# Kernel optimization log

Hardware: AMD Instinct MI355X
Metric: run time of the kernel (lower is better)

Reference implementation:

```python
import jax, jax.numpy as jnp
import numpy as np

D_MODEL = 512
NUM_HEADS = 8
DEPTH = D_MODEL // NUM_HEADS
MAX_SEQ = 2048
B, L = 4, 1024


def setup_inputs() -> dict:
    key = jax.random.key(0)
    ks = jax.random.split(key, 13)
    s = 0.02
    return {
        "v": jax.random.normal(ks[0], (B, L, D_MODEL), jnp.float32),
        "k": jax.random.normal(ks[1], (B, L, D_MODEL), jnp.float32),
        "q": jax.random.normal(ks[2], (B, L, D_MODEL), jnp.float32),
        "mask": jnp.zeros((1, 1, L, L), jnp.float32),
        "wq_w": jax.random.normal(ks[3], (D_MODEL, D_MODEL), jnp.float32) * s,
        "wq_b": jnp.zeros((D_MODEL,), jnp.float32),
        "wk_w": jax.random.normal(ks[4], (D_MODEL, D_MODEL), jnp.float32) * s,
        "wk_b": jnp.zeros((D_MODEL,), jnp.float32),
        "wv_w": jax.random.normal(ks[5], (D_MODEL, D_MODEL), jnp.float32) * s,
        "wv_b": jnp.zeros((D_MODEL,), jnp.float32),
        "wo_w": jax.random.normal(ks[6], (D_MODEL, D_MODEL), jnp.float32) * s,
        "wo_b": jnp.zeros((D_MODEL,), jnp.float32),
        "pos_emb": jax.random.normal(ks[7], (MAX_SEQ, DEPTH), jnp.float32) * s,
    }


def _split_heads(x, batch):
    # [B, L, d_model] -> [B, H, L, depth]
    return x.reshape(batch, -1, NUM_HEADS, DEPTH).transpose(0, 2, 1, 3)


def reference(v, k, q, mask, wq_w, wq_b, wk_w, wk_b, wv_w, wv_b, wo_w, wo_b, pos_emb):
    batch, l_q, _ = q.shape
    qh = _split_heads(q @ wq_w + wq_b, batch)   # [B,H,Lq,depth]
    kh = _split_heads(k @ wk_w + wk_b, batch)   # [B,H,Lk,depth]
    vh = _split_heads(v @ wv_w + wv_b, batch)   # [B,H,Lk,depth]
    l_k = kh.shape[2]

    # relative position embedding slice: last l_q rows of pos_emb -> [Lq, depth]
    e = pos_emb[max(0, MAX_SEQ - l_q):, :]
    qe = jnp.einsum('nhld,md->nhlm', qh, e)     # [B,H,Lq,Lq]

    # upper-left triangular masking: keep entries with i + j >= Lq - 1
    keep = (jnp.arange(l_q)[:, None] + jnp.arange(l_q)[None, :]) >= (l_q - 1)
    qe = qe * keep.astype(qe.dtype)

    # skew trick: pad left on last dim, reshape [L, L+1]->[L+1, L], drop first row
    padded = jnp.pad(qe, ((0, 0), (0, 0), (0, 0), (1, 0)))
    srel = padded.reshape(batch, NUM_HEADS, l_q + 1, l_q)[:, :, 1:, :]  # [B,H,Lq,Lq]
    if l_k > l_q:
        srel = jnp.pad(srel, ((0, 0), (0, 0), (0, 0), (0, l_k - l_q)))
    elif l_k < l_q:
        srel = srel[..., :l_k]

    scale = 1.0 / jnp.sqrt(jnp.asarray(DEPTH, qh.dtype))
    logits = (jnp.einsum('nhld,nhmd->nhlm', qh, kh) + srel) * scale
    logits = logits + mask * (-1e9)
    attn = jax.nn.softmax(logits, axis=-1)      # [B,H,Lq,Lk]
    ctx = jnp.einsum('nhlm,nhmd->nhld', attn, vh)
    ctx = ctx.transpose(0, 2, 1, 3).reshape(batch, l_q, D_MODEL)
    out = ctx @ wo_w + wo_b
    return out, attn
```

## Files before the change

### kernel.cpp

```cpp
#include <hip/hip_runtime.h>

typedef __attribute__((ext_vector_type(4))) float f32x4;
typedef __attribute__((ext_vector_type(8))) short s16x8;
typedef __attribute__((ext_vector_type(4))) unsigned short u16x4;

__device__ inline unsigned short f2bf(float f) {
  unsigned int u = __builtin_bit_cast(unsigned int, f);
  u += 0x7fff + ((u >> 16) & 1);
  return (unsigned short)(u >> 16);
}
__device__ inline float bf2f(unsigned short u) {
  return __builtin_bit_cast(float, (unsigned int)u << 16);
}

__device__ __forceinline__ void async16(const void* g, void* s) {
  __builtin_amdgcn_global_load_lds(
      (const __attribute__((address_space(1))) unsigned int*)g,
      (__attribute__((address_space(3))) unsigned int*)s, 16, 0, 0);
}

__global__ __launch_bounds__(256) void cast_kernel(
    const float* __restrict__ v, const float* __restrict__ k, const float* __restrict__ q,
    const float* __restrict__ wq, const float* __restrict__ wk, const float* __restrict__ wv,
    const float* __restrict__ wo, const float* __restrict__ pos,
    unsigned short* __restrict__ qbf, unsigned short* __restrict__ kbf,
    unsigned short* __restrict__ vbf, unsigned short* __restrict__ wqT,
    unsigned short* __restrict__ wkT, unsigned short* __restrict__ wvT,
    unsigned short* __restrict__ woT, unsigned short* __restrict__ ebf) {
  int seg = blockIdx.y;
  int tid = blockIdx.x * blockDim.x + threadIdx.x;
  int stride = gridDim.x * blockDim.x;
  if (seg < 3) {
    const float* src = seg == 0 ? q : (seg == 1 ? k : v);
    unsigned short* dst = seg == 0 ? qbf : (seg == 1 ? kbf : vbf);
    for (int i = tid; i < 4096 * 512 / 4; i += stride) {
      f32x4 x = *(const f32x4*)&src[i * 4];
      u16x4 o = {f2bf(x[0]), f2bf(x[1]), f2bf(x[2]), f2bf(x[3])};
      *(u16x4*)&dst[i * 4] = o;
    }
  } else if (seg < 7) {
    const float* src = seg == 3 ? wq : seg == 4 ? wk : seg == 5 ? wv : wo;
    unsigned short* dst = seg == 3 ? wqT : seg == 4 ? wkT : seg == 5 ? wvT : woT;
    for (int i = tid; i < 512 * 128; i += stride) {
      int n = i >> 7, k0 = (i & 127) * 4;
      u16x4 o = {f2bf(src[(k0 + 0) * 512 + n]), f2bf(src[(k0 + 1) * 512 + n]),
                 f2bf(src[(k0 + 2) * 512 + n]), f2bf(src[(k0 + 3) * 512 + n])};
      *(u16x4*)&dst[n * 512 + k0] = o;
    }
  } else {
    for (int i = tid; i < 1024 * 64 / 4; i += stride) {
      f32x4 x = *(const f32x4*)&pos[1024 * 64 + i * 4];
      u16x4 o = {f2bf(x[0]), f2bf(x[1]), f2bf(x[2]), f2bf(x[3])};
      *(u16x4*)&ebf[i * 4] = o;
    }
  }
}

__device__ __forceinline__ void gemm_main(
    const unsigned short* __restrict__ A, const unsigned short* __restrict__ Bt,
    unsigned short* As, unsigned short* Bs, int r0, int c0, int tid,
    f32x4 acc[4][4]) {
  int lane = tid & 63, w = tid >> 6;
  int wr = w >> 1, wc = w & 1;
  int frow = lane & 15, kg = lane >> 4;
  for (int k0 = 0; k0 < 512; k0 += 32) {
#pragma unroll
    for (int j = 0; j < 2; ++j) {
      int t = tid + j * 256;
      int row = t >> 2, col = (t & 3) * 8;
      *(s16x8*)&As[row * 32 + col] = *(const s16x8*)&A[(size_t)(r0 + row) * 512 + k0 + col];
      *(s16x8*)&Bs[row * 32 + col] = *(const s16x8*)&Bt[(size_t)(c0 + row) * 512 + k0 + col];
    }
    __syncthreads();
    s16x8 af[4], bfr[4];
#pragma unroll
    for (int mi = 0; mi < 4; ++mi) af[mi] = *(s16x8*)&As[(wr * 64 + mi * 16 + frow) * 32 + kg * 8];
#pragma unroll
    for (int ni = 0; ni < 4; ++ni) bfr[ni] = *(s16x8*)&Bs[(wc * 64 + ni * 16 + frow) * 32 + kg * 8];
#pragma unroll
    for (int mi = 0; mi < 4; ++mi)
#pragma unroll
      for (int ni = 0; ni < 4; ++ni)
        acc[mi][ni] = __builtin_amdgcn_mfma_f32_16x16x32_bf16(af[mi], bfr[ni], acc[mi][ni], 0, 0, 0);
    __syncthreads();
  }
}

__global__ __launch_bounds__(256, 2) void proj3_kernel(
    const unsigned short* __restrict__ qbf, const unsigned short* __restrict__ kbf,
    const unsigned short* __restrict__ vbf, const unsigned short* __restrict__ wqT,
    const unsigned short* __restrict__ wkT, const unsigned short* __restrict__ wvT,
    const float* __restrict__ wq_b, const float* __restrict__ wk_b,
    const float* __restrict__ wv_b, unsigned short* __restrict__ qhw,
    unsigned short* __restrict__ khw, unsigned short* __restrict__ vhT) {
  __shared__ unsigned short As[128 * 32];
  __shared__ unsigned short Bs[128 * 32];
  int z = blockIdx.z;
  const unsigned short* A = z == 0 ? qbf : z == 1 ? kbf : vbf;
  const unsigned short* Bt = z == 0 ? wqT : z == 1 ? wkT : wvT;
  const float* bias = z == 0 ? wq_b : z == 1 ? wk_b : wv_b;
  unsigned short* outp = z == 0 ? qhw : z == 1 ? khw : vhT;
  int r0 = blockIdx.x * 128, c0 = blockIdx.y * 128;
  int tid = threadIdx.x;
  int lane = tid & 63, w = tid >> 6;
  int wr = w >> 1, wc = w & 1;
  int frow = lane & 15, kg = lane >> 4;
  f32x4 acc[4][4] = {};
  gemm_main(A, Bt, As, Bs, r0, c0, tid, acc);
#pragma unroll
  for (int ni = 0; ni < 4; ++ni) {
    int gc = c0 + wc * 64 + ni * 16 + frow;
    float bi = bias[gc];
#pragma unroll
    for (int mi = 0; mi < 4; ++mi) {
#pragma unroll
      for (int reg = 0; reg < 4; ++reg) {
        int gr = r0 + wr * 64 + mi * 16 + kg * 4 + reg;
        float val = acc[mi][ni][reg] + bi;
        if (z != 2) {
          outp[(size_t)((gr >> 10) * 8 + (gc >> 6)) * 65536 +
               (size_t)(gr & 1023) * 64 + (gc & 63)] = f2bf(val);
        } else {
          outp[(size_t)((gr >> 10) * 8 + (gc >> 6)) * 65536 +
               (size_t)(gc & 63) * 1024 + (gr & 1023)] = f2bf(val);
        }
      }
    }
  }
}

__global__ __launch_bounds__(256, 2) void gemm_out_kernel(
    const unsigned short* __restrict__ A, const unsigned short* __restrict__ Bt,
    const float* __restrict__ bias, float* __restrict__ outp) {
  __shared__ unsigned short As[128 * 32];
  __shared__ unsigned short Bs[128 * 32];
  int r0 = blockIdx.x * 128, c0 = blockIdx.y * 128;
  int tid = threadIdx.x;
  int lane = tid & 63, w = tid >> 6;
  int wr = w >> 1, wc = w & 1;
  int frow = lane & 15, kg = lane >> 4;
  f32x4 acc[4][4] = {};
  gemm_main(A, Bt, As, Bs, r0, c0, tid, acc);
#pragma unroll
  for (int ni = 0; ni < 4; ++ni) {
    int gc = c0 + wc * 64 + ni * 16 + frow;
    float bi = bias[gc];
#pragma unroll
    for (int mi = 0; mi < 4; ++mi)
#pragma unroll
      for (int reg = 0; reg < 4; ++reg) {
        int gr = r0 + wr * 64 + mi * 16 + kg * 4 + reg;
        outp[(size_t)gr * 512 + gc] = acc[mi][ni][reg] + bi;
      }
  }
}

__global__ __launch_bounds__(256, 2) void attn_kernel(
    const unsigned short* __restrict__ qh, const unsigned short* __restrict__ kh,
    const unsigned short* __restrict__ vhT, const unsigned short* __restrict__ ebf,
    const float* __restrict__ mask, float* __restrict__ attn_out,
    unsigned short* __restrict__ ctx) {
  __shared__ unsigned short S[16 * 1024];
  __shared__ unsigned short KV[2][8192];
  __shared__ float redmax[4][16], redsum[4][16];
  int nh = blockIdx.y;
  int l0 = blockIdx.x * 16;
  int tid = threadIdx.x;
  int lane = tid & 63, w = tid >> 6;
  int frow = lane & 15, kg = lane >> 4;

  auto sp = [&](int r, int c) -> unsigned short* {
    int byte = (r << 11) + (c << 1);
    byte ^= (r & 7) << 4;
    return (unsigned short*)((char*)S + byte);
  };

  auto stageKE = [&](const unsigned short* srcbase, int buf) {
#pragma unroll
    for (int i = 0; i < 4; ++i) {
      int u = (w * 4 + i) * 64 + lane;
      int row = u >> 3, pp = u & 7;
      async16(srcbase + (size_t)row * 64 + (size_t)((pp ^ (row & 7)) * 8),
              &KV[buf][(w * 4 + i) * 512]);
    }
  };
  auto stageV = [&](const unsigned short* srcbase, int c, int buf) {
#pragma unroll
    for (int i = 0; i < 4; ++i) {
      int u = (w * 4 + i) * 64 + lane;
      int row = u >> 4, pp = u & 15;
      int p = (pp & 8) | ((pp ^ (row & 7)) & 7);
      async16(srcbase + (size_t)row * 1024 + c * 128 + p * 8,
              &KV[buf][(w * 4 + i) * 512]);
    }
  };

  const unsigned short* qbase = qh + ((size_t)nh * 1024 + l0 + frow) * 64 + kg * 8;
  s16x8 qf0 = *(const s16x8*)(qbase);
  s16x8 qf1 = *(const s16x8*)(qbase + 32);

  int cmin = 1008 - l0;
  int cstart = cmin >> 7;
  stageKE(ebf + (size_t)cstart * 8192, cstart & 1);
  for (int c = cstart; c < 8; ++c) {
    int buf = c & 1;
    if (c < 7) {
      stageKE(ebf + (size_t)(c + 1) * 8192, buf ^ 1);
      asm volatile("s_waitcnt vmcnt(4)" ::: "memory");
    } else {
      asm volatile("s_waitcnt vmcnt(0)" ::: "memory");
    }
    __builtin_amdgcn_s_barrier();
    __builtin_amdgcn_sched_barrier(0);
#pragma unroll
    for (int tt = 0; tt < 2; ++tt) {
      int j0 = c * 128 + (w * 2 + tt) * 16;
      if (j0 + 15 < cmin) continue;
      int lr = (w * 2 + tt) * 16 + frow;
      const char* base = (const char*)&KV[buf][0] + lr * 128;
      s16x8 b0 = *(const s16x8*)(base + ((kg ^ (lr & 7)) << 4));
      s16x8 b1 = *(const s16x8*)(base + (((4 + kg) ^ (lr & 7)) << 4));
      f32x4 a = {};
      a = __builtin_amdgcn_mfma_f32_16x16x32_bf16(b0, qf0, a, 0, 0, 0);
      a = __builtin_amdgcn_mfma_f32_16x16x32_bf16(b1, qf1, a, 0, 0, 0);
      u16x4 pk = {f2bf(a[0]), f2bf(a[1]), f2bf(a[2]), f2bf(a[3])};
      *(u16x4*)sp(frow, j0 + kg * 4) = pk;
    }
    __builtin_amdgcn_s_barrier();
    __builtin_amdgcn_sched_barrier(0);
  }
  __syncthreads();

  f32x4 lg[16];
  stageKE(kh + (size_t)nh * 65536, 0);
#pragma unroll
  for (int c = 0; c < 8; ++c) {
    int buf = c & 1;
    if (c < 7) {
      stageKE(kh + (size_t)nh * 65536 + (size_t)(c + 1) * 8192, buf ^ 1);
      asm volatile("s_waitcnt vmcnt(4)" ::: "memory");
    } else {
      asm volatile("s_waitcnt vmcnt(0)" ::: "memory");
    }
    __builtin_amdgcn_s_barrier();
    __builtin_amdgcn_sched_barrier(0);
#pragma unroll
    for (int tt = 0; tt < 2; ++tt) {
      int lr = (w * 2 + tt) * 16 + frow;
      const char* base = (const char*)&KV[buf][0] + lr * 128;
      s16x8 b0 = *(const s16x8*)(base + ((kg ^ (lr & 7)) << 4));
      s16x8 b1 = *(const s16x8*)(base + (((4 + kg) ^ (lr & 7)) << 4));
      f32x4 a = {};
      a = __builtin_amdgcn_mfma_f32_16x16x32_bf16(b0, qf0, a, 0, 0, 0);
      a = __builtin_amdgcn_mfma_f32_16x16x32_bf16(b1, qf1, a, 0, 0, 0);
      lg[c * 2 + tt] = a;
    }
    __builtin_amdgcn_s_barrier();
    __builtin_amdgcn_sched_barrier(0);
  }

  int lq = l0 + frow;
#pragma unroll
  for (int c = 0; c < 8; ++c) {
#pragma unroll
    for (int tt = 0; tt < 2; ++tt) {
      int t = c * 2 + tt;
      int m0k = c * 128 + (w * 2 + tt) * 16 + kg * 4;
      f32x4 mk = *(const f32x4*)&mask[(size_t)lq * 1024 + m0k];
#pragma unroll
      for (int reg = 0; reg < 4; ++reg) {
        int m = m0k + reg;
        float srel = (m <= lq) ? bf2f(*sp(frow, 1023 + m - lq)) : 0.f;
        lg[t][reg] = (lg[t][reg] + srel) * 0.125f + mk[reg] * -1e9f;
      }
    }
  }

  f32x4 vmax = lg[0];
#pragma unroll
  for (int t = 1; t < 16; ++t) {
#pragma unroll
    for (int reg = 0; reg < 4; ++reg) vmax[reg] = fmaxf(vmax[reg], lg[t][reg]);
  }
  float mx = fmaxf(fmaxf(vmax[0], vmax[1]), fmaxf(vmax[2], vmax[3]));
  mx = fmaxf(mx, __shfl_xor(mx, 16));
  mx = fmaxf(mx, __shfl_xor(mx, 32));
  float s = 0.f;
#pragma unroll
  for (int t = 0; t < 16; ++t) {
#pragma unroll
    for (int reg = 0; reg < 4; ++reg) {
      lg[t][reg] = __expf(lg[t][reg] - mx);
      s += lg[t][reg];
    }
  }
  s += __shfl_xor(s, 16);
  s += __shfl_xor(s, 32);
  if (lane < 16) {
    redmax[w][lane] = mx;
    redsum[w][lane] = s;
  }
  __syncthreads();

  float gmax = fmaxf(fmaxf(redmax[0][frow], redmax[1][frow]),
                     fmaxf(redmax[2][frow], redmax[3][frow]));
  float gsum = redsum[0][frow] * __expf(redmax[0][frow] - gmax) +
               redsum[1][frow] * __expf(redmax[1][frow] - gmax) +
               redsum[2][frow] * __expf(redmax[2][frow] - gmax) +
               redsum[3][frow] * __expf(redmax[3][frow] - gmax);
  float fac = __expf(mx - gmax) / gsum;

  size_t arow = ((size_t)nh * 1024 + lq) * 1024;
#pragma unroll
  for (int c = 0; c < 8; ++c) {
#pragma unroll
    for (int tt = 0; tt < 2; ++tt) {
      int t = c * 2 + tt;
      int m0k = c * 128 + (w * 2 + tt) * 16 + kg * 4;
      f32x4 pn;
#pragma unroll
      for (int reg = 0; reg < 4; ++reg) pn[reg] = lg[t][reg] * fac;
      *(f32x4*)&attn_out[arow + m0k] = pn;
      u16x4 pb = {f2bf(pn[0]), f2bf(pn[1]), f2bf(pn[2]), f2bf(pn[3])};
      *(u16x4*)sp(frow, m0k) = pb;
    }
  }
  __syncthreads();

  {
    f32x4 acc = {};
    int rd = w * 16 + frow;
    const unsigned short* vsrc = vhT + (size_t)nh * 65536;
    stageV(vsrc, 0, 0);
#pragma unroll
    for (int c = 0; c < 8; ++c) {
      int buf = c & 1;
      if (c < 7) {
        stageV(vsrc, c + 1, buf ^ 1);
        asm volatile("s_waitcnt vmcnt(4)" ::: "memory");
      } else {
        asm volatile("s_waitcnt vmcnt(0)" ::: "memory");
      }
      __builtin_amdgcn_s_barrier();
      __builtin_amdgcn_sched_barrier(0);
#pragma unroll
      for (int ks = 0; ks < 4; ++ks) {
        s16x8 a = *(s16x8*)sp(frow, c * 128 + ks * 32 + kg * 8);
        int part = ks * 4 + kg;
        int partp = (part & 8) | ((part ^ (rd & 7)) & 7);
        s16x8 b = *(const s16x8*)((const char*)&KV[buf][0] + rd * 256 + partp * 16);
        acc = __builtin_amdgcn_mfma_f32_16x16x32_bf16(a, b, acc, 0, 0, 0);
      }
      __builtin_amdgcn_s_barrier();
      __builtin_amdgcn_sched_barrier(0);
    }
    int n = nh >> 3, h = nh & 7;
#pragma unroll
    for (int reg = 0; reg < 4; ++reg) {
      int rr = kg * 4 + reg;
      ctx[((size_t)(n * 1024 + l0 + rr)) * 512 + h * 64 + w * 16 + frow] = f2bf(acc[reg]);
    }
  }
}

extern "C" void kernel_launch(void* const* d_in, const int* in_sizes, int n_in,
                              void* d_out, int out_size, void* d_ws, size_t ws_size,
                              hipStream_t stream) {
  const float* v = (const float*)d_in[0];
  const float* k = (const float*)d_in[1];
  const float* q = (const float*)d_in[2];
  const float* mask = (const float*)d_in[3];
  const float* wq_w = (const float*)d_in[4];
  const float* wq_b = (const float*)d_in[5];
  const float* wk_w = (const float*)d_in[6];
  const float* wk_b = (const float*)d_in[7];
  const float* wv_w = (const float*)d_in[8];
  const float* wv_b = (const float*)d_in[9];
  const float* wo_w = (const float*)d_in[10];
  const float* wo_b = (const float*)d_in[11];
  const float* pos = (const float*)d_in[12];

  float* outp = (float*)d_out;
  float* attn_out = outp + (size_t)4 * 1024 * 512;

  char* ws = (char*)d_ws;
  unsigned short* qbf = (unsigned short*)(ws);
  unsigned short* kbf = (unsigned short*)(ws + ((size_t)4 << 20));
  unsigned short* vbf = (unsigned short*)(ws + ((size_t)8 << 20));
  unsigned short* wqT = (unsigned short*)(ws + ((size_t)12 << 20));
  unsigned short* wkT = (unsigned short*)(ws + ((size_t)12 << 20) + (512 << 10));
  unsigned short* wvT = (unsigned short*)(ws + ((size_t)13 << 20));
  unsigned short* woT = (unsigned short*)(ws + ((size_t)13 << 20) + (512 << 10));
  unsigned short* ebf = (unsigned short*)(ws + ((size_t)14 << 20));
  unsigned short* qhw = (unsigned short*)(ws + ((size_t)16 << 20));
  unsigned short* khw = (unsigned short*)(ws + ((size_t)20 << 20));
  unsigned short* vhT = (unsigned short*)(ws + ((size_t)24 << 20));
  unsigned short* ctx = qbf;

  cast_kernel<<<dim3(256, 8), 256, 0, stream>>>(v, k, q, wq_w, wk_w, wv_w, wo_w, pos,
                                                qbf, kbf, vbf, wqT, wkT, wvT, woT, ebf);
  proj3_kernel<<<dim3(32, 4, 3), 256, 0, stream>>>(qbf, kbf, vbf, wqT, wkT, wvT,
                                                   wq_b, wk_b, wv_b, qhw, khw, vhT);
  attn_kernel<<<dim3(64, 32), 256, 0, stream>>>(qhw, khw, vhT, ebf, mask, attn_out, ctx);
  gemm_out_kernel<<<dim3(32, 4), 256, 0, stream>>>(ctx, woT, wo_b, outp);
}
```

Baseline: 135.5 us.

## Drop per-chunk workgroup barriers and prefetch K/E/V chunks further ahead

In the three double-buffered staging loops (relative-embedding, K and V), each wave appears to stage and read only its own rows of the shared buffer. On that basis the per-iteration s_barrier pairs are replaced with per-wave waitcnt fences. The next-chunk load is now issued after the current chunk's LDS reads finish, so two chunks are in flight. The first two V chunks are also issued before the softmax/normalisation phase so that load latency overlaps that work. The risk is a data race if any wave reads LDS rows staged by another wave, since no barrier now orders them.

```diff
diff --git a/kernel.cpp b/kernel.cpp
--- a/kernel.cpp
+++ b/kernel.cpp
@@ -202,15 +202,11 @@
   int cmin = 1008 - l0;
   int cstart = cmin >> 7;
   stageKE(ebf + (size_t)cstart * 8192, cstart & 1);
+  if (cstart + 1 < 8) stageKE(ebf + (size_t)(cstart + 1) * 8192, (cstart + 1) & 1);
   for (int c = cstart; c < 8; ++c) {
     int buf = c & 1;
-    if (c < 7) {
-      stageKE(ebf + (size_t)(c + 1) * 8192, buf ^ 1);
-      asm volatile("s_waitcnt vmcnt(4)" ::: "memory");
-    } else {
-      asm volatile("s_waitcnt vmcnt(0)" ::: "memory");
-    }
-    __builtin_amdgcn_s_barrier();
+    if (c + 1 < 8) { asm volatile("s_waitcnt vmcnt(4)" ::: "memory"); }
+    else           { asm volatile("s_waitcnt vmcnt(0)" ::: "memory"); }
     __builtin_amdgcn_sched_barrier(0);
 #pragma unroll
     for (int tt = 0; tt < 2; ++tt) {
@@ -226,23 +222,21 @@
       u16x4 pk = {f2bf(a[0]), f2bf(a[1]), f2bf(a[2]), f2bf(a[3])};
       *(u16x4*)sp(frow, j0 + kg * 4) = pk;
     }
-    __builtin_amdgcn_s_barrier();
+    asm volatile("s_waitcnt lgkmcnt(0)" ::: "memory");
     __builtin_amdgcn_sched_barrier(0);
+    if (c + 2 < 8) stageKE(ebf + (size_t)(c + 2) * 8192, buf);
   }
   __syncthreads();
 
   f32x4 lg[16];
-  stageKE(kh + (size_t)nh * 65536, 0);
+  const unsigned short* kbase = kh + (size_t)nh * 65536;
+  stageKE(kbase, 0);
+  stageKE(kbase + 8192, 1);
 #pragma unroll
   for (int c = 0; c < 8; ++c) {
     int buf = c & 1;
-    if (c < 7) {
-      stageKE(kh + (size_t)nh * 65536 + (size_t)(c + 1) * 8192, buf ^ 1);
-      asm volatile("s_waitcnt vmcnt(4)" ::: "memory");
-    } else {
-      asm volatile("s_waitcnt vmcnt(0)" ::: "memory");
-    }
-    __builtin_amdgcn_s_barrier();
+    if (c + 1 < 8) { asm volatile("s_waitcnt vmcnt(4)" ::: "memory"); }
+    else           { asm volatile("s_waitcnt vmcnt(0)" ::: "memory"); }
     __builtin_amdgcn_sched_barrier(0);
 #pragma unroll
     for (int tt = 0; tt < 2; ++tt) {
@@ -255,9 +249,14 @@
       a = __builtin_amdgcn_mfma_f32_16x16x32_bf16(b1, qf1, a, 0, 0, 0);
       lg[c * 2 + tt] = a;
     }
-    __builtin_amdgcn_s_barrier();
+    asm volatile("s_waitcnt lgkmcnt(0)" ::: "memory");
     __builtin_amdgcn_sched_barrier(0);
-  }
+    if (c + 2 < 8) stageKE(kbase + (size_t)(c + 2) * 8192, buf);
+  }
+
+  const unsigned short* vsrc = vhT + (size_t)nh * 65536;
+  stageV(vsrc, 0, 0);
+  stageV(vsrc, 1, 1);
 
   int lq = l0 + frow;
 #pragma unroll
@@ -330,18 +329,11 @@
   {
     f32x4 acc = {};
     int rd = w * 16 + frow;
-    const unsigned short* vsrc = vhT + (size_t)nh * 65536;
-    stageV(vsrc, 0, 0);
 #pragma unroll
     for (int c = 0; c < 8; ++c) {
       int buf = c & 1;
-      if (c < 7) {
-        stageV(vsrc, c + 1, buf ^ 1);
-        asm volatile("s_waitcnt vmcnt(4)" ::: "memory");
-      } else {
-        asm volatile("s_waitcnt vmcnt(0)" ::: "memory");
-      }
-      __builtin_amdgcn_s_barrier();
+      if (c + 1 < 8) { asm volatile("s_waitcnt vmcnt(4)" ::: "memory"); }
+      else           { asm volatile("s_waitcnt vmcnt(0)" ::: "memory"); }
       __builtin_amdgcn_sched_barrier(0);
 #pragma unroll
       for (int ks = 0; ks < 4; ++ks) {
@@ -351,8 +343,9 @@
         s16x8 b = *(const s16x8*)((const char*)&KV[buf][0] + rd * 256 + partp * 16);
         acc = __builtin_amdgcn_mfma_f32_16x16x32_bf16(a, b, acc, 0, 0, 0);
       }
-      __builtin_amdgcn_s_barrier();
+      asm volatile("s_waitcnt lgkmcnt(0)" ::: "memory");
       __builtin_amdgcn_sched_barrier(0);
+      if (c + 2 < 8) stageV(vsrc, c + 2, buf);
     }
     int n = nh >> 3, h = nh & 7;
 #pragma unroll
```

New measurement: 130.3 us. 3.8% less time.
